# Performance work log

Hardware: AMD Instinct MI355X
Metric: run time of the kernel (lower is better)

Reference implementation:

```python
import jax, jax.numpy as jnp
import numpy as np
import math

E, H, L = 32, 4, 3            # embed_dim, num_heads, n_cross_blocks
PEP_LEN, MHC_LEN, VOCAB, B = 15, 74, 22, 8192
EPS = 1e-5


def _pe(max_len, d):
    pos = np.arange(max_len)[:, None].astype(np.float32)
    div = np.exp(np.arange(0, d, 2).astype(np.float32) * (-math.log(10000.0) / d))
    pe = np.zeros((max_len, d), np.float32)
    pe[:, 0::2] = np.sin(pos * div)
    pe[:, 1::2] = np.cos(pos * div)
    return jnp.asarray(pe)


def _ln(x, g, b):
    m = x.mean(-1, keepdims=True)
    v = jnp.var(x, axis=-1, keepdims=True)
    return (x - m) / jnp.sqrt(v + EPS) * g + b


def _bn(x, g, b):  # BatchNorm1d in training mode (batch stats, biased var)
    m = x.mean(0)
    v = jnp.var(x, axis=0)
    return (x - m) / jnp.sqrt(v + EPS) * g + b


def _mha(q, k, v, inw, inb, ow, ob):
    # torch nn.MultiheadAttention: its own in_proj on (q,k,v) then out_proj
    Bq, S, E_ = q.shape
    Sk = k.shape[1]
    Dh = E_ // H
    wq, wk, wv = inw[:E_], inw[E_:2 * E_], inw[2 * E_:]
    bq, bk, bv = inb[:E_], inb[E_:2 * E_], inb[2 * E_:]
    qh = (q @ wq.T + bq).reshape(Bq, S, H, Dh)
    kh = (k @ wk.T + bk).reshape(Bq, Sk, H, Dh)
    vh = (v @ wv.T + bv).reshape(Bq, Sk, H, Dh)
    sc = jnp.einsum('bqhd,bkhd->bhqk', qh, kh) / jnp.sqrt(jnp.asarray(Dh, q.dtype))
    o = jnp.einsum('bhqk,bkhd->bqhd', jax.nn.softmax(sc, -1), vh).reshape(Bq, S, E_)
    return o @ ow.T + ob


def _forward(x_pep, cmhc, emb, ln_g, ln_b, pre_qkv_w, pre_qkv_b, sa_inw, sa_inb,
             sa_ow, sa_ob, cpre_qkv_w, cpre_qkv_b, ca_inw, ca_inb, ca_ow, ca_ob,
             fc_w, fc_b, proj_w, proj_b, h1_w1, h1_b1, h1_bn_g, h1_bn_b, h1_w2,
             h1_b2, h2_bn1_g, h2_bn1_b, h2_w1, h2_b1, h2_bn2_g, h2_bn2_b, h2_w2, h2_b2):
    x = jnp.tanh(emb[x_pep] + _pe(PEP_LEN, E)[None])  # Embedding + PE + Tanh
    for l in range(L):  # 3 CrossBlocks
        x = _ln(x, ln_g[l, 0], ln_b[l, 0])
        q = x @ pre_qkv_w[l, 0].T + pre_qkv_b[l, 0]
        k = x @ pre_qkv_w[l, 1].T + pre_qkv_b[l, 1]
        v = x @ pre_qkv_w[l, 2].T + pre_qkv_b[l, 2]
        x = x + _mha(q, k, v, sa_inw[l], sa_inb[l], sa_ow[l], sa_ob[l])
        x = _ln(x, ln_g[l, 1], ln_b[l, 1])
        cq = x @ cpre_qkv_w[l, 0].T + cpre_qkv_b[l, 0]
        ck = cmhc @ cpre_qkv_w[l, 1].T + cpre_qkv_b[l, 1]
        cv = cmhc @ cpre_qkv_w[l, 2].T + cpre_qkv_b[l, 2]
        x = x + _mha(cq, ck, cv, ca_inw[l], ca_inb[l], ca_ow[l], ca_ob[l])
        x = _ln(x, ln_g[l, 2], ln_b[l, 2])
        h = jax.nn.gelu(x @ fc_w[l].T + fc_b[l], approximate=False)
        x = x + h @ proj_w[l].T + proj_b[l]
    t = x[:, 0, :]  # CLS token
    a = jax.nn.relu(t @ h1_w1.T + h1_b1)
    a = _bn(a, h1_bn_g, h1_bn_b)
    a = jax.nn.relu(a @ h1_w2.T + h1_b2)
    s = t + a
    s = _bn(s, h2_bn1_g, h2_bn1_b)
    s = jax.nn.relu(s @ h2_w1.T + h2_b1)
    s = _bn(s, h2_bn2_g, h2_bn2_b)
    return jax.nn.sigmoid(s @ h2_w2.T + h2_b2)  # [B, 1]


def setup_inputs() -> dict:
    key = jax.random.key(0)
    ks = iter(jax.random.split(key, 64))

    def rn(shape, scale=0.02):
        return jax.random.normal(next(ks), shape, jnp.float32) * scale

    d = {}
    d['x_pep'] = jax.random.randint(next(ks), (B, PEP_LEN), 0, VOCAB)
    d['cmhc'] = jax.random.normal(next(ks), (B, MHC_LEN, E), jnp.float32)
    d['emb'] = rn((VOCAB, E), 1.0)
    d['ln_g'] = jnp.ones((L, 3, E)); d['ln_b'] = jnp.zeros((L, 3, E))
    d['pre_qkv_w'] = rn((L, 3, E, E)); d['pre_qkv_b'] = jnp.zeros((L, 3, E))
    d['sa_inw'] = rn((L, 3 * E, E)); d['sa_inb'] = jnp.zeros((L, 3 * E))
    d['sa_ow'] = rn((L, E, E)); d['sa_ob'] = jnp.zeros((L, E))
    d['cpre_qkv_w'] = rn((L, 3, E, E)); d['cpre_qkv_b'] = jnp.zeros((L, 3, E))
    d['ca_inw'] = rn((L, 3 * E, E)); d['ca_inb'] = jnp.zeros((L, 3 * E))
    d['ca_ow'] = rn((L, E, E)); d['ca_ob'] = jnp.zeros((L, E))
    d['fc_w'] = rn((L, 4 * E, E)); d['fc_b'] = jnp.zeros((L, 4 * E))
    d['proj_w'] = rn((L, E, 4 * E)); d['proj_b'] = jnp.zeros((L, E))
    d['h1_w1'] = rn((128, E)); d['h1_b1'] = jnp.zeros((128,))
    d['h1_bn_g'] = jnp.ones((128,)); d['h1_bn_b'] = jnp.zeros((128,))
    d['h1_w2'] = rn((E, 128)); d['h1_b2'] = jnp.zeros((E,))
    d['h2_bn1_g'] = jnp.ones((E,)); d['h2_bn1_b'] = jnp.zeros((E,))
    d['h2_w1'] = rn((8, E)); d['h2_b1'] = jnp.zeros((8,))
    d['h2_bn2_g'] = jnp.ones((8,)); d['h2_bn2_b'] = jnp.zeros((8,))
    d['h2_w2'] = rn((1, 8)); d['h2_b2'] = jnp.zeros((1,))
    return d


def reference(x_pep, cmhc, emb, ln_g, ln_b, pre_qkv_w, pre_qkv_b, sa_inw, sa_inb,
              sa_ow, sa_ob, cpre_qkv_w, cpre_qkv_b, ca_inw, ca_inb, ca_ow, ca_ob,
              fc_w, fc_b, proj_w, proj_b, h1_w1, h1_b1, h1_bn_g, h1_bn_b, h1_w2,
              h1_b2, h2_bn1_g, h2_bn1_b, h2_w1, h2_b1, h2_bn2_g, h2_bn2_b, h2_w2, h2_b2):
    return _forward(x_pep, cmhc, emb, ln_g, ln_b, pre_qkv_w, pre_qkv_b, sa_inw, sa_inb,
                    sa_ow, sa_ob, cpre_qkv_w, cpre_qkv_b, ca_inw, ca_inb, ca_ow, ca_ob,
                    fc_w, fc_b, proj_w, proj_b, h1_w1, h1_b1, h1_bn_g, h1_bn_b, h1_w2,
                    h1_b2, h2_bn1_g, h2_bn1_b, h2_w1, h2_b1, h2_bn2_g, h2_bn2_b, h2_w2, h2_b2)
```

## Files before the change

kernel.cpp:

```cpp
#include <hip/hip_runtime.h>
#include <math.h>

#define E32   32
#define Hh    4
#define Lh    3
#define SP    15
#define SM    74
#define EPSF  1e-5f

#define WSYNC() do { __builtin_amdgcn_wave_barrier(); asm volatile("" ::: "memory"); } while (0)

#define XS_STRIDE 36
#define OO_STRIDE 36
#define HB_STRIDE 132
#define SAMP_LDS  2528

__global__ void fuse_weights(const float* pre_w, const float* pre_b,
                             const float* sa_inw, const float* sa_inb,
                             const float* cpre_w, const float* cpre_b,
                             const float* ca_inw, const float* ca_inb,
                             float* fw, float* fb, float* pe) {
    int id = blockIdx.x;
    if (id == 18) {
        for (int i = threadIdx.x; i < SP * 32; i += blockDim.x) {
            int s = i >> 5, e = i & 31;
            float div = expf(-(float)(e & ~1) * 0.28782313662425572f);
            float ang = (float)s * div;
            pe[i] = (e & 1) ? cosf(ang) : sinf(ang);
        }
        return;
    }
    int l = id / 6, which = id % 6;
    int j = which % 3;
    bool cross = which >= 3;
    float scale = (j == 1) ? 0.35355339059327373f : 1.f;
    const float* A  = (cross ? ca_inw : sa_inw) + l * 96 * 32 + j * 32 * 32;
    const float* ab = (cross ? ca_inb : sa_inb) + l * 96 + j * 32;
    const float* P  = (cross ? cpre_w : pre_w) + (l * 3 + j) * 1024;
    const float* pb = (cross ? cpre_b : pre_b) + (l * 3 + j) * 32;
    float* W = fw + id * 1024;
    float* b = fb + id * 32;
    for (int i = threadIdx.x; i < 1024; i += blockDim.x) {
        int e = i >> 5, k = i & 31;
        float acc = 0.f;
        #pragma unroll
        for (int m = 0; m < 32; ++m) acc += A[e * 32 + m] * P[m * 32 + k];
        W[i] = acc * scale;
    }
    for (int e = threadIdx.x; e < 32; e += blockDim.x) {
        float acc = ab[e];
        #pragma unroll
        for (int m = 0; m < 32; ++m) acc += A[e * 32 + m] * pb[m];
        b[e] = acc * scale;
    }
}


__device__ inline void wave_ln(float* xs, const float* g, const float* bia, int l) {
    int s = l >> 2, q = l & 3;
    float v[8];
    if (s < SP) {
        const float* row = xs + s * XS_STRIDE + q * 8;
        #pragma unroll
        for (int i = 0; i < 8; ++i) v[i] = row[i];
    } else {
        #pragma unroll
        for (int i = 0; i < 8; ++i) v[i] = 0.f;
    }
    float m = 0.f, m2 = 0.f;
    #pragma unroll
    for (int i = 0; i < 8; ++i) { m += v[i]; m2 += v[i] * v[i]; }
    m += __shfl_xor(m, 1);  m2 += __shfl_xor(m2, 1);
    m += __shfl_xor(m, 2);  m2 += __shfl_xor(m2, 2);
    m *= (1.f / 32.f);
    float var = m2 * (1.f / 32.f) - m * m;
    float r = rsqrtf(var + EPSF);
    if (s < SP) {
        float* row = xs + s * XS_STRIDE + q * 8;
        #pragma unroll
        for (int i = 0; i < 8; ++i)
            row[i] = (v[i] - m) * r * g[q * 8 + i] + bia[q * 8 + i];
    }
}

template <int SK>
__device__ inline void wave_attn(const float* xs, const float* xk, int ldk,
                                 const float* Wq, const float* bq,
                                 const float* Wk, const float* bk,
                                 const float* Wv, const float* bv,
                                 float* oo, int l) {
    int qi = l & 15, h = l >> 4;
    int qs = (qi < SP) ? qi : SP - 1;
    const float* xq = xs + qs * XS_STRIDE;

    float q8[8];
    #pragma unroll
    for (int d = 0; d < 8; ++d) {
        const float* wr = Wq + (h * 8 + d) * 32;
        float acc = bq[h * 8 + d];
        #pragma unroll
        for (int k = 0; k < 32; ++k) acc += xq[k] * wr[k];
        q8[d] = acc;
    }
    float z[32];
    #pragma unroll
    for (int k = 0; k < 32; ++k) z[k] = 0.f;
    float alpha = 0.f;
    #pragma unroll
    for (int d = 0; d < 8; ++d) {
        const float* wr = Wk + (h * 8 + d) * 32;
        float qd = q8[d];
        alpha += qd * bk[h * 8 + d];
        #pragma unroll
        for (int k = 0; k < 32; ++k) z[k] += qd * wr[k];
    }

    float pc[32];
    #pragma unroll
    for (int k = 0; k < 32; ++k) pc[k] = 0.f;
    float M = -3.0e38f, S = 0.f;
    for (int j = 0; j < SK; ++j) {
        const float* xr = xk + j * ldk;
        float sc_ = alpha;
        #pragma unroll
        for (int k = 0; k < 32; ++k) sc_ += z[k] * xr[k];
        float t = fmaxf(M, sc_);
        float a = expf(M - t);
        float p = expf(sc_ - t);
        S = S * a + p;
        #pragma unroll
        for (int k = 0; k < 32; ++k) pc[k] = pc[k] * a + p * xr[k];
        M = t;
    }
    float rinv = 1.f / S;
    #pragma unroll
    for (int k = 0; k < 32; ++k) pc[k] *= rinv;

    float o8[8];
    #pragma unroll
    for (int d = 0; d < 8; ++d) {
        const float* wr = Wv + (h * 8 + d) * 32;
        float acc = bv[h * 8 + d];
        #pragma unroll
        for (int k = 0; k < 32; ++k) acc += pc[k] * wr[k];
        o8[d] = acc;
    }
    if (qi < SP) {
        float* orow = oo + qi * OO_STRIDE + h * 8;
        #pragma unroll
        for (int d = 0; d < 8; ++d) orow[d] = o8[d];
    }
}

__device__ inline void wave_outproj(const float* oo, const float* W, const float* bo,
                                    float* xs, int l) {
    int e = l & 31, hi = l >> 5;
    float wrow[32];
    const float* wr = W + e * 32;
    #pragma unroll
    for (int k = 0; k < 32; ++k) wrow[k] = wr[k];
    float be = bo[e];
    #pragma unroll
    for (int j = 0; j < 8; ++j) {
        int s = j * 2 + hi;
        if (s < SP) {
            const float* orow = oo + s * OO_STRIDE;
            float acc = be;
            #pragma unroll
            for (int k = 0; k < 32; ++k) acc += orow[k] * wrow[k];
            xs[s * XS_STRIDE + e] += acc;
        }
    }
}

__global__ __launch_bounds__(256, 4) void pan_main(
    const int* x_pep, const float* cmhc, const float* emb,
    const float* ln_g, const float* ln_b,
    const float* sa_ow, const float* sa_ob,
    const float* ca_ow, const float* ca_ob,
    const float* fc_w, const float* fc_b,
    const float* proj_w, const float* proj_b,
    const float* fw, const float* fb, const float* pe_tab,
    float* t_out, int nB)
{
    __shared__ float lds[4 * SAMP_LDS];
    const int w = threadIdx.x >> 6;
    const int l = threadIdx.x & 63;
    const int b = blockIdx.x * 4 + w;
    if (b >= nB) return;
    float* xs = lds + w * SAMP_LDS;
    float* sc = xs + 544;

    {
        const int* tok = x_pep + b * SP;
        #pragma unroll
        for (int j = 0; j < 8; ++j) {
            int i = j * 64 + l;
            if (i < SP * 32) {
                int s = i >> 5, e = i & 31;
                xs[s * XS_STRIDE + e] = tanhf(emb[tok[s] * 32 + e] + pe_tab[i]);
            }
        }
    }
    WSYNC();

    const float* cm = cmhc + (size_t)b * SM * 32;

    for (int ly = 0; ly < Lh; ++ly) {
        const float* fwl = fw + ly * 6 * 1024;
        const float* fbl = fb + ly * 6 * 32;

        wave_ln(xs, ln_g + (ly * 3 + 0) * 32, ln_b + (ly * 3 + 0) * 32, l);
        WSYNC();
        wave_attn<SP>(xs, xs, XS_STRIDE,
                      fwl + 0 * 1024, fbl + 0 * 32,
                      fwl + 1 * 1024, fbl + 1 * 32,
                      fwl + 2 * 1024, fbl + 2 * 32, sc, l);
        WSYNC();
        wave_outproj(sc, sa_ow + ly * 1024, sa_ob + ly * 32, xs, l);
        WSYNC();

        wave_ln(xs, ln_g + (ly * 3 + 1) * 32, ln_b + (ly * 3 + 1) * 32, l);
        WSYNC();
        wave_attn<SM>(xs, cm, 32,
                      fwl + 3 * 1024, fbl + 3 * 32,
                      fwl + 4 * 1024, fbl + 4 * 32,
                      fwl + 5 * 1024, fbl + 5 * 32, sc, l);
        WSYNC();
        wave_outproj(sc, ca_ow + ly * 1024, ca_ob + ly * 32, xs, l);
        WSYNC();

        wave_ln(xs, ln_g + (ly * 3 + 2) * 32, ln_b + (ly * 3 + 2) * 32, l);
        WSYNC();
        #pragma unroll
        for (int half = 0; half < 2; ++half) {
            int f = half * 64 + l;
            const float* wr = fc_w + ly * 4096 + f * 32;
            float wrow[32];
            #pragma unroll
            for (int k = 0; k < 32; ++k) wrow[k] = wr[k];
            float bf = fc_b[ly * 128 + f];
            for (int s = 0; s < SP; ++s) {
                const float* xrow = xs + s * XS_STRIDE;
                float acc = bf;
                #pragma unroll
                for (int k = 0; k < 32; ++k) acc += xrow[k] * wrow[k];
                sc[s * HB_STRIDE + f] =
                    acc * 0.5f * (1.f + erff(acc * 0.70710678118654752f));
            }
        }
        WSYNC();
        {
            int e = l & 31, hi = l >> 5;
            float acc[8];
            float be = proj_b[ly * 32 + e];
            #pragma unroll
            for (int j = 0; j < 8; ++j) acc[j] = be;
            #pragma unroll
            for (int c = 0; c < 4; ++c) {
                const float* wr = proj_w + ly * 4096 + e * 128 + c * 32;
                float wrow[32];
                #pragma unroll
                for (int k = 0; k < 32; ++k) wrow[k] = wr[k];
                #pragma unroll
                for (int j = 0; j < 8; ++j) {
                    int s = j * 2 + hi;
                    if (s < SP) {
                        const float* hrow = sc + s * HB_STRIDE + c * 32;
                        #pragma unroll
                        for (int k = 0; k < 32; ++k) acc[j] += hrow[k] * wrow[k];
                    }
                }
            }
            #pragma unroll
            for (int j = 0; j < 8; ++j) {
                int s = j * 2 + hi;
                if (s < SP) xs[s * XS_STRIDE + e] += acc[j];
            }
        }
        WSYNC();
    }

    if (l < 32) t_out[(size_t)b * 32 + l] = xs[l];
}

__global__ __launch_bounds__(256) void head1(const float* t_in, const float* w1,
                                             const float* b1, float* a1,
                                             double* stats, int nB) {
    __shared__ float tb[64 * 32];
    __shared__ float wtf[32 * 129];
    __shared__ float bsh[128];
    __shared__ float rs[128], rss[128];
    int t = threadIdx.x;
    int r0 = blockIdx.x * 64;
    for (int i = t; i < 64 * 32; i += 256) tb[i] = t_in[r0 * 32 + i];
    for (int i = t; i < 128 * 32; i += 256) {
        int f = i >> 5, k = i & 31;
        wtf[k * 129 + f] = w1[i];
    }
    if (t < 128) bsh[t] = b1[t];
    __syncthreads();
    int f = t & 127;
    float ls = 0.f, lss = 0.f;
    for (int rr = t >> 7; rr < 64; rr += 2) {
        float acc = bsh[f];
        #pragma unroll
        for (int k = 0; k < 32; ++k) acc += tb[rr * 32 + k] * wtf[k * 129 + f];
        acc = fmaxf(acc, 0.f);
        a1[(size_t)(r0 + rr) * 128 + f] = acc;
        ls += acc; lss += acc * acc;
    }
    if (t >= 128) { rs[f] = ls; rss[f] = lss; }
    __syncthreads();
    if (t < 128) {
        atomicAdd(&stats[f], (double)(ls + rs[f]));
        atomicAdd(&stats[128 + f], (double)(lss + rss[f]));
    }
}

__global__ __launch_bounds__(256) void head2(const float* t_in, const float* a1,
                                             const float* g, const float* bb,
                                             const float* w2, const float* b2,
                                             float* sbuf, const double* stats,
                                             double* stats2, int nB) {
    __shared__ float scale[128], shift[128];
    __shared__ float wt2[128 * 33];
    __shared__ float rs[256], rss[256];
    int t = threadIdx.x;
    if (t < 128) {
        double m = stats[t] / (double)nB;
        double var = stats[128 + t] / (double)nB - m * m;
        float sc = g[t] * rsqrtf((float)var + EPSF);
        scale[t] = sc;
        shift[t] = bb[t] - (float)m * sc;
    }
    for (int i = t; i < 32 * 128; i += 256) {
        int e = i >> 7, k = i & 127;
        wt2[k * 33 + e] = w2[i];
    }
    __syncthreads();
    int r0 = blockIdx.x * 64;
    int e = t & 31;
    float ls = 0.f, lss = 0.f;
    for (int rr = t >> 5; rr < 64; rr += 8) {
        const float* arow = a1 + (size_t)(r0 + rr) * 128;
        float acc = b2[e];
        #pragma unroll 8
        for (int k = 0; k < 128; ++k)
            acc += (arow[k] * scale[k] + shift[k]) * wt2[k * 33 + e];
        acc = fmaxf(acc, 0.f);
        float sv = t_in[(size_t)(r0 + rr) * 32 + e] + acc;
        sbuf[(size_t)(r0 + rr) * 32 + e] = sv;
        ls += sv; lss += sv * sv;
    }
    rs[t] = ls; rss[t] = lss;
    __syncthreads();
    if (t < 32) {
        float s1 = 0.f, s2 = 0.f;
        for (int j = 0; j < 8; ++j) { s1 += rs[t + 32 * j]; s2 += rss[t + 32 * j]; }
        atomicAdd(&stats2[t], (double)s1);
        atomicAdd(&stats2[32 + t], (double)s2);
    }
}

__global__ __launch_bounds__(256) void head3(const float* sbuf, const float* g,
                                             const float* bb, const float* w,
                                             const float* b, float* rbuf,
                                             const double* stats2, double* stats3,
                                             int nB) {
    __shared__ float scale[32], shift[32];
    __shared__ float wsh[8 * 32];
    __shared__ float rs[256], rss[256];
    int t = threadIdx.x;
    if (t < 32) {
        double m = stats2[t] / (double)nB;
        double var = stats2[32 + t] / (double)nB - m * m;
        float sc = g[t] * rsqrtf((float)var + EPSF);
        scale[t] = sc;
        shift[t] = bb[t] - (float)m * sc;
    }
    if (t < 8 * 32) wsh[t] = w[t];
    __syncthreads();
    int r0 = blockIdx.x * 64;
    int f = t & 7;
    float ls = 0.f, lss = 0.f;
    for (int rr = t >> 3; rr < 64; rr += 32) {
        const float* srow = sbuf + (size_t)(r0 + rr) * 32;
        float acc = b[f];
        #pragma unroll
        for (int k = 0; k < 32; ++k)
            acc += (srow[k] * scale[k] + shift[k]) * wsh[f * 32 + k];
        acc = fmaxf(acc, 0.f);
        rbuf[(size_t)(r0 + rr) * 8 + f] = acc;
        ls += acc; lss += acc * acc;
    }
    rs[t] = ls; rss[t] = lss;
    __syncthreads();
    if (t < 8) {
        float s1 = 0.f, s2 = 0.f;
        for (int j = 0; j < 32; ++j) { s1 += rs[t + 8 * j]; s2 += rss[t + 8 * j]; }
        atomicAdd(&stats3[t], (double)s1);
        atomicAdd(&stats3[8 + t], (double)s2);
    }
}

__global__ __launch_bounds__(256) void head4(const float* rbuf, const float* g,
                                             const float* bb, const float* w2,
                                             const float* b2, float* out,
                                             const double* stats3, int nB) {
    __shared__ float scale[8], shift[8], wv[8];
    int t = threadIdx.x;
    if (t < 8) {
        double m = stats3[t] / (double)nB;
        double var = stats3[8 + t] / (double)nB - m * m;
        float sc = g[t] * rsqrtf((float)var + EPSF);
        scale[t] = sc;
        shift[t] = bb[t] - (float)m * sc;
        wv[t] = w2[t];
    }
    __syncthreads();
    int i = blockIdx.x * 256 + t;
    if (i < nB) {
        const float* rr = rbuf + (size_t)i * 8;
        float acc = b2[0];
        #pragma unroll
        for (int k = 0; k < 8; ++k) acc += (rr[k] * scale[k] + shift[k]) * wv[k];
        out[i] = 1.f / (1.f + expf(-acc));
    }
}

extern "C" void kernel_launch(void* const* d_in, const int* in_sizes, int n_in,
                              void* d_out, int out_size, void* d_ws, size_t ws_size,
                              hipStream_t stream) {
    const int*   x_pep  = (const int*)  d_in[0];
    const float* cmhc   = (const float*)d_in[1];
    const float* emb    = (const float*)d_in[2];
    const float* ln_g   = (const float*)d_in[3];
    const float* ln_b   = (const float*)d_in[4];
    const float* pre_w  = (const float*)d_in[5];
    const float* pre_b  = (const float*)d_in[6];
    const float* sa_inw = (const float*)d_in[7];
    const float* sa_inb = (const float*)d_in[8];
    const float* sa_ow  = (const float*)d_in[9];
    const float* sa_ob  = (const float*)d_in[10];
    const float* cpre_w = (const float*)d_in[11];
    const float* cpre_b = (const float*)d_in[12];
    const float* ca_inw = (const float*)d_in[13];
    const float* ca_inb = (const float*)d_in[14];
    const float* ca_ow  = (const float*)d_in[15];
    const float* ca_ob  = (const float*)d_in[16];
    const float* fc_w   = (const float*)d_in[17];
    const float* fc_b   = (const float*)d_in[18];
    const float* proj_w = (const float*)d_in[19];
    const float* proj_b = (const float*)d_in[20];
    const float* h1_w1  = (const float*)d_in[21];
    const float* h1_b1  = (const float*)d_in[22];
    const float* h1_g   = (const float*)d_in[23];
    const float* h1_bb  = (const float*)d_in[24];
    const float* h1_w2  = (const float*)d_in[25];
    const float* h1_b2  = (const float*)d_in[26];
    const float* h2_g1  = (const float*)d_in[27];
    const float* h2_bb1 = (const float*)d_in[28];
    const float* h2_w1  = (const float*)d_in[29];
    const float* h2_b1  = (const float*)d_in[30];
    const float* h2_g2  = (const float*)d_in[31];
    const float* h2_bb2 = (const float*)d_in[32];
    const float* h2_w2  = (const float*)d_in[33];
    const float* h2_b2  = (const float*)d_in[34];
    float* out = (float*)d_out;

    const int nB = in_sizes[0] / SP;

    float* wsf   = (float*)d_ws;
    float* fw    = wsf;
    float* fb    = fw + 18 * 1024;
    float* pe    = fb + 18 * 32;
    float* t_buf = pe + 480;
    float* a1    = t_buf + (size_t)nB * 32;
    float* sbuf  = a1 + (size_t)nB * 128;
    float* rbuf  = sbuf + (size_t)nB * 32;
    uintptr_t sp = (uintptr_t)(rbuf + (size_t)nB * 8);
    sp = (sp + 7) & ~(uintptr_t)7;
    double* stats  = (double*)sp;
    double* stats2 = stats + 256;
    double* stats3 = stats2 + 64;

    hipMemsetAsync(stats, 0, 336 * sizeof(double), stream);

    fuse_weights<<<19, 256, 0, stream>>>(pre_w, pre_b, sa_inw, sa_inb,
                                         cpre_w, cpre_b, ca_inw, ca_inb,
                                         fw, fb, pe);

    pan_main<<<(nB + 3) / 4, 256, 0, stream>>>(x_pep, cmhc, emb, ln_g, ln_b,
                                               sa_ow, sa_ob, ca_ow, ca_ob,
                                               fc_w, fc_b, proj_w, proj_b,
                                               fw, fb, pe, t_buf, nB);

    head1<<<nB / 64, 256, 0, stream>>>(t_buf, h1_w1, h1_b1, a1, stats, nB);
    head2<<<nB / 64, 256, 0, stream>>>(t_buf, a1, h1_g, h1_bb, h1_w2, h1_b2,
                                       sbuf, stats, stats2, nB);
    head3<<<nB / 64, 256, 0, stream>>>(sbuf, h2_g1, h2_bb1, h2_w1, h2_b1,
                                       rbuf, stats2, stats3, nB);
    head4<<<(nB + 255) / 256, 256, 0, stream>>>(rbuf, h2_g2, h2_bb2, h2_w2, h2_b2,
                                                out, stats3, nB);
}
```

Before: 1.448 ms.

## Split MLP hidden into halves to shrink LDS, use 4-way dot products

The FFN hidden buffer is processed in two 64-wide halves, with fc and proj interleaved per half. This cuts per-sample LDS from 2528 to 1504 floats, which allows more blocks per CU. Dot products are split into four independent accumulators to shorten FMA dependency chains, and the q/o projection arrays are computed inline. Launch bounds drop the min-blocks hint from 4 to 3, loosening register pressure, and the split adds an extra wave barrier per half.

```diff
diff --git a/kernel.cpp b/kernel.cpp
--- a/kernel.cpp
+++ b/kernel.cpp
@@ -12,8 +12,8 @@
 
 #define XS_STRIDE 36
 #define OO_STRIDE 36
-#define HB_STRIDE 132
-#define SAMP_LDS  2528
+#define SC_FLOATS 960
+#define SAMP_LDS  1504
 
 __global__ void fuse_weights(const float* pre_w, const float* pre_b,
                              const float* sa_inw, const float* sa_inb,
@@ -56,6 +56,18 @@
 }
 
 
+__device__ inline float dot32(const float* a, const float* b) {
+    float p0 = 0.f, p1 = 0.f, p2 = 0.f, p3 = 0.f;
+    #pragma unroll
+    for (int k = 0; k < 32; k += 4) {
+        p0 += a[k] * b[k];
+        p1 += a[k + 1] * b[k + 1];
+        p2 += a[k + 2] * b[k + 2];
+        p3 += a[k + 3] * b[k + 3];
+    }
+    return (p0 + p1) + (p2 + p3);
+}
+
 __device__ inline void wave_ln(float* xs, const float* g, const float* bia, int l) {
     int s = l >> 2, q = l & 3;
     float v[8];
@@ -93,23 +105,14 @@
     int qs = (qi < SP) ? qi : SP - 1;
     const float* xq = xs + qs * XS_STRIDE;
 
-    float q8[8];
-    #pragma unroll
-    for (int d = 0; d < 8; ++d) {
-        const float* wr = Wq + (h * 8 + d) * 32;
-        float acc = bq[h * 8 + d];
-        #pragma unroll
-        for (int k = 0; k < 32; ++k) acc += xq[k] * wr[k];
-        q8[d] = acc;
-    }
     float z[32];
     #pragma unroll
     for (int k = 0; k < 32; ++k) z[k] = 0.f;
     float alpha = 0.f;
     #pragma unroll
     for (int d = 0; d < 8; ++d) {
+        float qd = bq[h * 8 + d] + dot32(xq, Wq + (h * 8 + d) * 32);
         const float* wr = Wk + (h * 8 + d) * 32;
-        float qd = q8[d];
         alpha += qd * bk[h * 8 + d];
         #pragma unroll
         for (int k = 0; k < 32; ++k) z[k] += qd * wr[k];
@@ -121,9 +124,7 @@
     float M = -3.0e38f, S = 0.f;
     for (int j = 0; j < SK; ++j) {
         const float* xr = xk + j * ldk;
-        float sc_ = alpha;
-        #pragma unroll
-        for (int k = 0; k < 32; ++k) sc_ += z[k] * xr[k];
+        float sc_ = alpha + dot32(z, xr);
         float t = fmaxf(M, sc_);
         float a = expf(M - t);
         float p = expf(sc_ - t);
@@ -136,19 +137,11 @@
     #pragma unroll
     for (int k = 0; k < 32; ++k) pc[k] *= rinv;
 
-    float o8[8];
-    #pragma unroll
-    for (int d = 0; d < 8; ++d) {
-        const float* wr = Wv + (h * 8 + d) * 32;
-        float acc = bv[h * 8 + d];
-        #pragma unroll
-        for (int k = 0; k < 32; ++k) acc += pc[k] * wr[k];
-        o8[d] = acc;
-    }
     if (qi < SP) {
         float* orow = oo + qi * OO_STRIDE + h * 8;
         #pragma unroll
-        for (int d = 0; d < 8; ++d) orow[d] = o8[d];
+        for (int d = 0; d < 8; ++d)
+            orow[d] = bv[h * 8 + d] + dot32(pc, Wv + (h * 8 + d) * 32);
     }
 }
 
@@ -165,15 +158,12 @@
         int s = j * 2 + hi;
         if (s < SP) {
             const float* orow = oo + s * OO_STRIDE;
-            float acc = be;
-            #pragma unroll
-            for (int k = 0; k < 32; ++k) acc += orow[k] * wrow[k];
-            xs[s * XS_STRIDE + e] += acc;
+            xs[s * XS_STRIDE + e] += be + dot32(orow, wrow);
         }
     }
 }
 
-__global__ __launch_bounds__(256, 4) void pan_main(
+__global__ __launch_bounds__(256, 3) void pan_main(
     const int* x_pep, const float* cmhc, const float* emb,
     const float* ln_g, const float* ln_b,
     const float* sa_ow, const float* sa_ob,
@@ -232,45 +222,43 @@
 
         wave_ln(xs, ln_g + (ly * 3 + 2) * 32, ln_b + (ly * 3 + 2) * 32, l);
         WSYNC();
-        #pragma unroll
-        for (int half = 0; half < 2; ++half) {
-            int f = half * 64 + l;
-            const float* wr = fc_w + ly * 4096 + f * 32;
-            float wrow[32];
-            #pragma unroll
-            for (int k = 0; k < 32; ++k) wrow[k] = wr[k];
-            float bf = fc_b[ly * 128 + f];
-            for (int s = 0; s < SP; ++s) {
-                const float* xrow = xs + s * XS_STRIDE;
-                float acc = bf;
-                #pragma unroll
-                for (int k = 0; k < 32; ++k) acc += xrow[k] * wrow[k];
-                sc[s * HB_STRIDE + f] =
-                    acc * 0.5f * (1.f + erff(acc * 0.70710678118654752f));
-            }
-        }
-        WSYNC();
         {
             int e = l & 31, hi = l >> 5;
             float acc[8];
             float be = proj_b[ly * 32 + e];
             #pragma unroll
             for (int j = 0; j < 8; ++j) acc[j] = be;
+
             #pragma unroll
-            for (int c = 0; c < 4; ++c) {
-                const float* wr = proj_w + ly * 4096 + e * 128 + c * 32;
-                float wrow[32];
-                #pragma unroll
-                for (int k = 0; k < 32; ++k) wrow[k] = wr[k];
-                #pragma unroll
-                for (int j = 0; j < 8; ++j) {
-                    int s = j * 2 + hi;
-                    if (s < SP) {
-                        const float* hrow = sc + s * HB_STRIDE + c * 32;
-                        #pragma unroll
-                        for (int k = 0; k < 32; ++k) acc[j] += hrow[k] * wrow[k];
+            for (int half = 0; half < 2; ++half) {
+                {
+                    int f = half * 64 + l;
+                    const float* wr = fc_w + ly * 4096 + f * 32;
+                    float wrow[32];
+                    #pragma unroll
+                    for (int k = 0; k < 32; ++k) wrow[k] = wr[k];
+                    float bf = fc_b[ly * 128 + f];
+                    for (int s = 0; s < SP; ++s) {
+                        float a = bf + dot32(xs + s * XS_STRIDE, wrow);
+                        sc[s * 64 + l] =
+                            a * 0.5f * (1.f + erff(a * 0.70710678118654752f));
                     }
                 }
+                WSYNC();
+                #pragma unroll
+                for (int c = 0; c < 2; ++c) {
+                    const float* wr = proj_w + ly * 4096 + e * 128 + half * 64 + c * 32;
+                    float wrow[32];
+                    #pragma unroll
+                    for (int k = 0; k < 32; ++k) wrow[k] = wr[k];
+                    #pragma unroll
+                    for (int j = 0; j < 8; ++j) {
+                        int s = j * 2 + hi;
+                        if (s < SP)
+                            acc[j] += dot32(sc + s * 64 + c * 32, wrow);
+                    }
+                }
+                WSYNC();
             }
             #pragma unroll
             for (int j = 0; j < 8; ++j) {
```

After: 5.358 ms. 3.7x slower.
